# Kernel optimization log

Hardware: AMD Instinct MI355X
Metric: run time of the kernel (lower is better)

Reference implementation:

```python
import jax, jax.numpy as jnp
import numpy as np

SCALE = 100.0  # sharp-softmax temperature from the torch module

def _build_tables():
    # ByteToNibbleFFN: W1 is identity(256) so it is mathematically a no-op; keep W2.
    W2_b2n = np.zeros((256, 32), np.float32)
    bb = np.arange(256)
    W2_b2n[bb, bb >> 4] = 1.0
    W2_b2n[bb, 16 + (bb & 15)] = 1.0
    # NibbleAddWithCarryFFN tables
    W1_add = np.zeros((34, 512), np.float32)
    W2_sum = np.zeros((512, 16), np.float32)
    W2_cout = np.zeros((512, 2), np.float32)
    for a in range(16):
        for b in range(16):
            for c in range(2):
                idx = a * 32 + b * 2 + c
                W1_add[a, idx] = 1.0
                W1_add[16 + b, idx] = 1.0
                W1_add[32 + c, idx] = 1.0
                t = a + b + c
                W2_sum[idx, t & 15] = 1.0
                W2_cout[idx, 1 if t > 15 else 0] = 1.0
    # NibbleToByteFFN tables
    W1_n2b = np.zeros((32, 256), np.float32)
    W2_n2b = np.zeros((256, 256), np.float32)
    for h in range(16):
        for l in range(16):
            addr = h * 16 + l
            W1_n2b[h, addr] = 1.0
            W1_n2b[16 + l, addr] = 1.0
            W2_n2b[addr, (h << 4) | l] = 1.0
    return tuple(jnp.asarray(t) for t in (W2_b2n, W1_add, W2_sum, W2_cout, W1_n2b, W2_n2b))

W2_B2N, W1_ADD, W2_SUM, W2_COUT, W1_N2B, W2_N2B = _build_tables()

def _b2n(x):
    # byte [.,256] -> (high [.,16], low [.,16]); W1=eye(256) omitted (identity)
    out = x @ W2_B2N
    return out[..., :16], out[..., 16:]

def _nib_add(a, b, cin):
    combined = jnp.concatenate([a, b, cin], axis=-1)           # [.,34]
    address = jax.nn.softmax(combined @ W1_ADD * SCALE, axis=-1)  # [.,512]
    return address @ W2_SUM, address @ W2_COUT

def _n2b(high, low):
    combined = jnp.concatenate([high, low], axis=-1)           # [.,32]
    address = jax.nn.softmax(combined @ W1_N2B * SCALE, axis=-1)  # [.,256]
    return address @ W2_N2B

def setup_inputs() -> dict:
    key = jax.random.key(0)
    k1, k2 = jax.random.split(key)
    B = 32768
    a = jax.random.uniform(k1, (B, 4, 256), dtype=jnp.float32)
    b = jax.random.uniform(k2, (B, 4, 256), dtype=jnp.float32)
    return {"a": a, "b": b}

def reference(a, b):
    # NeuralALU.add: ripple-carry add over 4 bytes, 2 nibble adds per byte
    B = a.shape[0]
    carry = jnp.zeros((B, 2), a.dtype).at[:, 0].set(1.0)  # carry_zero one-hot
    out_bytes = []
    for i in range(4):  # fixed structural loop over bytes (carry dependence)
        ah, al = _b2n(a[:, i])
        bh, bl = _b2n(b[:, i])
        sl, carry = _nib_add(al, bl, carry)
        sh, carry = _nib_add(ah, bh, carry)
        out_bytes.append(_n2b(sh, sl))
    return jnp.stack(out_bytes, axis=1)  # [B,4,256]
```

## Files before the change

### kernel.cpp

```cpp
#include <hip/hip_runtime.h>

#define NIB_SCALE 100.0f

template<int CTRL>
__device__ __forceinline__ float fdpp(float x) {
    return __int_as_float(__builtin_amdgcn_update_dpp(
        0, __float_as_int(x), CTRL, 0xF, 0xF, true));
}

__device__ __forceinline__ float rsum16d(float v) {
    v += fdpp<0x121>(v); v += fdpp<0x122>(v); v += fdpp<0x124>(v); v += fdpp<0x128>(v);
    return v;
}
__device__ __forceinline__ float rmax16d(float v) {
    v = fmaxf(v, fdpp<0x121>(v)); v = fmaxf(v, fdpp<0x122>(v));
    v = fmaxf(v, fdpp<0x124>(v)); v = fmaxf(v, fdpp<0x128>(v));
    return v;
}
__device__ __forceinline__ float scan16d(float v) {
    v += fdpp<0x111>(v); v += fdpp<0x112>(v); v += fdpp<0x114>(v); v += fdpp<0x118>(v);
    return v;
}
__device__ __forceinline__ float softmax16d(float v) {
    float m = rmax16d(v);
    float e = __expf(NIB_SCALE * (v - m));
    float s = rsum16d(e);
    return e / s;
}
__device__ __forceinline__ float sharp_sigmoid(float c) {
    return 1.0f / (1.0f + __expf(NIB_SCALE * (1.0f - 2.0f * c)));
}

__device__ __forceinline__ float conv_quad(float g0, float g1, float g2, float g3,
                                           const float4 q) {
    return fmaf(g0, q.x, fmaf(g1, q.y, fmaf(g2, q.z, g3 * q.w)));
}

#define COLSUM_CHUNK(dst, r4, c)                                  \
    {                                                             \
        float s0 = rsum16d(r4.x), s1 = rsum16d(r4.y);             \
        float s2 = rsum16d(r4.z), s3 = rsum16d(r4.w);             \
        float t0 = (k & 1) ? s1 : s0;                             \
        float t1 = (k & 1) ? s3 : s2;                             \
        float tc = (k & 2) ? t1 : t0;                             \
        dst = ((k >> 2) == (c)) ? tc : dst;                       \
    }

__device__ __forceinline__ void carry_chain(const float4 O16L, const float4 O15L,
                                            const float4 O16H, const float4 O15H, int b,
                                            float& pc0, float& pc1, float& qc0, float& qc1) {
    float qc1_0 = sharp_sigmoid(O16L.x);
    float qc0_0 = 1.f - qc1_0;
    float pc1_1 = sharp_sigmoid(qc0_0 * O16H.x + qc1_0 * O15H.x);
    float pc0_1 = 1.f - pc1_1;
    float qc1_1 = sharp_sigmoid(pc0_1 * O16L.y + pc1_1 * O15L.y);
    float qc0_1 = 1.f - qc1_1;
    float pc1_2 = sharp_sigmoid(qc0_1 * O16H.y + qc1_1 * O15H.y);
    float pc0_2 = 1.f - pc1_2;
    float qc1_2 = sharp_sigmoid(pc0_2 * O16L.z + pc1_2 * O15L.z);
    float qc0_2 = 1.f - qc1_2;
    float pc1_3 = sharp_sigmoid(qc0_2 * O16H.z + qc1_2 * O15H.z);
    float pc0_3 = 1.f - pc1_3;
    float qc1_3 = sharp_sigmoid(pc0_3 * O16L.w + pc1_3 * O15L.w);
    float qc0_3 = 1.f - qc1_3;
    pc0 = b == 0 ? 1.f   : b == 1 ? pc0_1 : b == 2 ? pc0_2 : pc0_3;
    pc1 = b == 0 ? 0.f   : b == 1 ? pc1_1 : b == 2 ? pc1_2 : pc1_3;
    qc0 = b == 0 ? qc0_0 : b == 1 ? qc0_1 : b == 2 ? qc0_2 : qc0_3;
    qc1 = b == 0 ? qc1_0 : b == 1 ? qc1_1 : b == 2 ? qc1_2 : qc1_3;
}

__global__ void nalu_kernel(const float* __restrict__ A,
                            const float* __restrict__ B,
                            float* __restrict__ O,
                            int nrows) {
    __shared__ __align__(16) float sQL[16][16];
    __shared__ __align__(16) float sQH[16][16];
    __shared__ __align__(16) float sPSL[16][16];
    __shared__ __align__(16) float sPSH[16][16];
    __shared__ __align__(16) float sOV[4][4][4];

    const int tid = threadIdx.x;
    const int k = tid & 15;
    const int g = tid >> 4;
    const int b = g & 3;
    const int w = tid >> 6;
    constexpr int ROWS = 4;
    const int row0 = blockIdx.x * (4 * ROWS) + w * ROWS;
    if (row0 >= nrows) return;
    long base = (long)row0 * 1024 + b * 256;

    const float4* pa4 = (const float4*)(A + base + 16 * k);
    const float4* pb4 = (const float4*)(B + base + 16 * k);
    float4 ra0 = pa4[0], ra1 = pa4[1], ra2 = pa4[2], ra3 = pa4[3];
    float4 rb0 = pb4[0], rb1 = pb4[1], rb2 = pb4[2], rb3 = pb4[3];

    #pragma unroll
    for (int i = 0; i < ROWS; ++i) {
        if (row0 + i >= nrows) break;
        const bool more = (i + 1 < ROWS) && (row0 + i + 1 < nrows);
        const long nbase = more ? base + 1024 : base;

        const float4* na4 = (const float4*)(A + nbase + 16 * k);
        const float4* nb4 = (const float4*)(B + nbase + 16 * k);
        float4 xa0 = na4[0], xa1 = na4[1], xa2 = na4[2], xa3 = na4[3];
        float4 xb0 = nb4[0], xb1 = nb4[1], xb2 = nb4[2], xb3 = nb4[3];

        float ah = ((ra0.x + ra0.y) + (ra0.z + ra0.w)) + ((ra1.x + ra1.y) + (ra1.z + ra1.w))
                 + ((ra2.x + ra2.y) + (ra2.z + ra2.w)) + ((ra3.x + ra3.y) + (ra3.z + ra3.w));
        float bh = ((rb0.x + rb0.y) + (rb0.z + rb0.w)) + ((rb1.x + rb1.y) + (rb1.z + rb1.w))
                 + ((rb2.x + rb2.y) + (rb2.z + rb2.w)) + ((rb3.x + rb3.y) + (rb3.z + rb3.w));
        float al = 0.f, bl = 0.f;
        COLSUM_CHUNK(al, ra0, 0) COLSUM_CHUNK(al, ra1, 1)
        COLSUM_CHUNK(al, ra2, 2) COLSUM_CHUNK(al, ra3, 3)
        COLSUM_CHUNK(bl, rb0, 0) COLSUM_CHUNK(bl, rb1, 1)
        COLSUM_CHUNK(bl, rb2, 2) COLSUM_CHUNK(bl, rb3, 3)

        __builtin_amdgcn_sched_barrier(0);

        float pal = softmax16d(al);
        float pbl = softmax16d(bl);
        float pah = softmax16d(ah);
        float pbh = softmax16d(bh);

        sQL[g][k] = pbl;
        sQH[g][k] = pbh;

        float mirl = fdpp<0x140>(pbl);
        float mirh = fdpp<0x140>(pbh);
        float T15l = scan16d(mirl);
        float T15h = scan16d(mirh);
        float ov15l = rsum16d(pal * T15l);
        float c15l  = rsum16d(pal * mirl);
        float ov15h = rsum16d(pah * T15h);
        float c15h  = rsum16d(pah * mirh);

        sOV[w][0][b] = ov15l - c15l;
        sOV[w][1][b] = ov15l;
        sOV[w][2][b] = ov15h - c15h;
        sOV[w][3][b] = ov15h;

        const float4 La = *(const float4*)&sQL[g][0];
        const float4 Lb = *(const float4*)&sQL[g][4];
        const float4 Lc = *(const float4*)&sQL[g][8];
        const float4 Ld = *(const float4*)&sQL[g][12];
        float rl = (conv_quad(pal,              fdpp<0x121>(pal), fdpp<0x122>(pal), fdpp<0x123>(pal), La)
                  + conv_quad(fdpp<0x124>(pal), fdpp<0x125>(pal), fdpp<0x126>(pal), fdpp<0x127>(pal), Lb))
                 + (conv_quad(fdpp<0x128>(pal), fdpp<0x129>(pal), fdpp<0x12A>(pal), fdpp<0x12B>(pal), Lc)
                  + conv_quad(fdpp<0x12C>(pal), fdpp<0x12D>(pal), fdpp<0x12E>(pal), fdpp<0x12F>(pal), Ld));

        const float4 Ha = *(const float4*)&sQH[g][0];
        const float4 Hb = *(const float4*)&sQH[g][4];
        const float4 Hc = *(const float4*)&sQH[g][8];
        const float4 Hd = *(const float4*)&sQH[g][12];
        float rh = (conv_quad(pah,              fdpp<0x121>(pah), fdpp<0x122>(pah), fdpp<0x123>(pah), Ha)
                  + conv_quad(fdpp<0x124>(pah), fdpp<0x125>(pah), fdpp<0x126>(pah), fdpp<0x127>(pah), Hb))
                 + (conv_quad(fdpp<0x128>(pah), fdpp<0x129>(pah), fdpp<0x12A>(pah), fdpp<0x12B>(pah), Hc)
                  + conv_quad(fdpp<0x12C>(pah), fdpp<0x12D>(pah), fdpp<0x12E>(pah), fdpp<0x12F>(pah), Hd));

        float pc0, pc1, qc0, qc1;
        carry_chain(*(const float4*)&sOV[w][0][0], *(const float4*)&sOV[w][1][0],
                    *(const float4*)&sOV[w][2][0], *(const float4*)&sOV[w][3][0],
                    b, pc0, pc1, qc0, qc1);

        float slow  = pc0 * rl + pc1 * fdpp<0x121>(rl);
        float shigh = qc0 * rh + qc1 * fdpp<0x121>(rh);

        float psl = softmax16d(slow);
        float psh = softmax16d(shigh);
        sPSL[g][k] = psl;
        sPSH[g][k] = psh;

        const float4 pslq = *(const float4*)&sPSL[g][4 * (k & 3)];
        float* po = O + base;
        #pragma unroll
        for (int c = 0; c < 4; ++c) {
            float hs = sPSH[g][4 * c + (k >> 2)];
            *(float4*)(po + 64 * c + 4 * k) =
                make_float4(hs * pslq.x, hs * pslq.y, hs * pslq.z, hs * pslq.w);
        }

        ra0 = xa0; ra1 = xa1; ra2 = xa2; ra3 = xa3;
        rb0 = xb0; rb1 = xb1; rb2 = xb2; rb3 = xb3;
        base = nbase;
    }
}

extern "C" void kernel_launch(void* const* d_in, const int* in_sizes, int n_in,
                              void* d_out, int out_size, void* d_ws, size_t ws_size,
                              hipStream_t stream) {
    const float* A = (const float*)d_in[0];
    const float* B = (const float*)d_in[1];
    float* O = (float*)d_out;
    int nrows = in_sizes[0] / 1024;
    int grid = (nrows + 15) / 16;
    nalu_kernel<<<grid, 256, 0, stream>>>(A, B, O, nrows);
}
```

Baseline: 315.1 us.

## Process two rows per wave with upfront loads, readlane carry chain, direct low-nibble sums

Each wave now handles two rows, and all loads for both rows are issued before any compute, in place of a four-row software-pipelined loop. The low-nibble sums are read with strided scalar loads instead of DPP column reductions, and the carry-chain inputs are broadcast with readlane instead of a shared-memory round trip. The final softmax uses a fixed max of 0.5 rather than a computed max, and occupancy is pinned to four waves per EU. This trades extra global load instructions and a numerically riskier softmax for less cross-lane reduction and LDS traffic.

```diff
diff --git a/kernel.cpp b/kernel.cpp
--- a/kernel.cpp
+++ b/kernel.cpp
@@ -27,8 +27,16 @@
     float s = rsum16d(e);
     return e / s;
 }
+__device__ __forceinline__ float softmax16_fix(float v) {
+    float e = __expf(NIB_SCALE * (v - 0.5f));
+    float s = rsum16d(e);
+    return e / s;
+}
 __device__ __forceinline__ float sharp_sigmoid(float c) {
     return 1.0f / (1.0f + __expf(NIB_SCALE * (1.0f - 2.0f * c)));
+}
+__device__ __forceinline__ float rdlane(float x, int l) {
+    return __int_as_float(__builtin_amdgcn_readlane(__float_as_int(x), l));
 }
 
 __device__ __forceinline__ float conv_quad(float g0, float g1, float g2, float g3,
@@ -36,153 +44,160 @@
     return fmaf(g0, q.x, fmaf(g1, q.y, fmaf(g2, q.z, g3 * q.w)));
 }
 
-#define COLSUM_CHUNK(dst, r4, c)                                  \
-    {                                                             \
-        float s0 = rsum16d(r4.x), s1 = rsum16d(r4.y);             \
-        float s2 = rsum16d(r4.z), s3 = rsum16d(r4.w);             \
-        float t0 = (k & 1) ? s1 : s0;                             \
-        float t1 = (k & 1) ? s3 : s2;                             \
-        float tc = (k & 2) ? t1 : t0;                             \
-        dst = ((k >> 2) == (c)) ? tc : dst;                       \
+__device__ __forceinline__ void stream_tail(float al, float bl, float ah, float bh,
+                                            int k, int g, int b,
+                                            float (&QL)[16][16], float (&QH)[16][16],
+                                            float (&PSL)[16][16], float (&PSH)[16][16],
+                                            float* __restrict__ po) {
+    float pal = softmax16d(al);
+    float pbl = softmax16d(bl);
+    float pah = softmax16d(ah);
+    float pbh = softmax16d(bh);
+
+    QL[g][k] = pbl;
+    QH[g][k] = pbh;
+
+    float mirl = fdpp<0x140>(pbl);
+    float mirh = fdpp<0x140>(pbh);
+    float T15l = scan16d(mirl);
+    float T15h = scan16d(mirh);
+    float ov15l = rsum16d(pal * T15l);
+    float c15l  = rsum16d(pal * mirl);
+    float ov15h = rsum16d(pah * T15h);
+    float c15h  = rsum16d(pah * mirh);
+    float ov16l = ov15l - c15l;
+    float ov16h = ov15h - c15h;
+
+    float l16[4] = { rdlane(ov16l,0), rdlane(ov16l,16), rdlane(ov16l,32), rdlane(ov16l,48) };
+    float l15[4] = { rdlane(ov15l,0), rdlane(ov15l,16), rdlane(ov15l,32), rdlane(ov15l,48) };
+    float h16[4] = { rdlane(ov16h,0), rdlane(ov16h,16), rdlane(ov16h,32), rdlane(ov16h,48) };
+    float h15[4] = { rdlane(ov15h,0), rdlane(ov15h,16), rdlane(ov15h,32), rdlane(ov15h,48) };
+
+    const float4 La = *(const float4*)&QL[g][0];
+    const float4 Lb = *(const float4*)&QL[g][4];
+    const float4 Lc = *(const float4*)&QL[g][8];
+    const float4 Ld = *(const float4*)&QL[g][12];
+    float rl = (conv_quad(pal,              fdpp<0x121>(pal), fdpp<0x122>(pal), fdpp<0x123>(pal), La)
+              + conv_quad(fdpp<0x124>(pal), fdpp<0x125>(pal), fdpp<0x126>(pal), fdpp<0x127>(pal), Lb))
+             + (conv_quad(fdpp<0x128>(pal), fdpp<0x129>(pal), fdpp<0x12A>(pal), fdpp<0x12B>(pal), Lc)
+              + conv_quad(fdpp<0x12C>(pal), fdpp<0x12D>(pal), fdpp<0x12E>(pal), fdpp<0x12F>(pal), Ld));
+
+    const float4 Ha = *(const float4*)&QH[g][0];
+    const float4 Hb = *(const float4*)&QH[g][4];
+    const float4 Hc = *(const float4*)&QH[g][8];
+    const float4 Hd = *(const float4*)&QH[g][12];
+    float rh = (conv_quad(pah,              fdpp<0x121>(pah), fdpp<0x122>(pah), fdpp<0x123>(pah), Ha)
+              + conv_quad(fdpp<0x124>(pah), fdpp<0x125>(pah), fdpp<0x126>(pah), fdpp<0x127>(pah), Hb))
+             + (conv_quad(fdpp<0x128>(pah), fdpp<0x129>(pah), fdpp<0x12A>(pah), fdpp<0x12B>(pah), Hc)
+              + conv_quad(fdpp<0x12C>(pah), fdpp<0x12D>(pah), fdpp<0x12E>(pah), fdpp<0x12F>(pah), Hd));
+
+    float qc1_0 = sharp_sigmoid(l16[0]);
+    float qc0_0 = 1.f - qc1_0;
+    float pc1_1 = sharp_sigmoid(qc0_0 * h16[0] + qc1_0 * h15[0]);
+    float pc0_1 = 1.f - pc1_1;
+    float qc1_1 = sharp_sigmoid(pc0_1 * l16[1] + pc1_1 * l15[1]);
+    float qc0_1 = 1.f - qc1_1;
+    float pc1_2 = sharp_sigmoid(qc0_1 * h16[1] + qc1_1 * h15[1]);
+    float pc0_2 = 1.f - pc1_2;
+    float qc1_2 = sharp_sigmoid(pc0_2 * l16[2] + pc1_2 * l15[2]);
+    float qc0_2 = 1.f - qc1_2;
+    float pc1_3 = sharp_sigmoid(qc0_2 * h16[2] + qc1_2 * h15[2]);
+    float pc0_3 = 1.f - pc1_3;
+    float qc1_3 = sharp_sigmoid(pc0_3 * l16[3] + pc1_3 * l15[3]);
+    float qc0_3 = 1.f - qc1_3;
+
+    float pc0 = b == 0 ? 1.f   : b == 1 ? pc0_1 : b == 2 ? pc0_2 : pc0_3;
+    float pc1 = b == 0 ? 0.f   : b == 1 ? pc1_1 : b == 2 ? pc1_2 : pc1_3;
+    float qc0 = b == 0 ? qc0_0 : b == 1 ? qc0_1 : b == 2 ? qc0_2 : qc0_3;
+    float qc1 = b == 0 ? qc1_0 : b == 1 ? qc1_1 : b == 2 ? qc1_2 : qc1_3;
+
+    float slow  = pc0 * rl + pc1 * fdpp<0x121>(rl);
+    float shigh = qc0 * rh + qc1 * fdpp<0x121>(rh);
+
+    float psl = softmax16_fix(slow);
+    float psh = softmax16_fix(shigh);
+    PSL[g][k] = psl;
+    PSH[g][k] = psh;
+
+    const float4 pslq = *(const float4*)&PSL[g][4 * (k & 3)];
+    #pragma unroll
+    for (int c = 0; c < 4; ++c) {
+        float hs = PSH[g][4 * c + (k >> 2)];
+        *(float4*)(po + 64 * c + 4 * k) =
+            make_float4(hs * pslq.x, hs * pslq.y, hs * pslq.z, hs * pslq.w);
     }
-
-__device__ __forceinline__ void carry_chain(const float4 O16L, const float4 O15L,
-                                            const float4 O16H, const float4 O15H, int b,
-                                            float& pc0, float& pc1, float& qc0, float& qc1) {
-    float qc1_0 = sharp_sigmoid(O16L.x);
-    float qc0_0 = 1.f - qc1_0;
-    float pc1_1 = sharp_sigmoid(qc0_0 * O16H.x + qc1_0 * O15H.x);
-    float pc0_1 = 1.f - pc1_1;
-    float qc1_1 = sharp_sigmoid(pc0_1 * O16L.y + pc1_1 * O15L.y);
-    float qc0_1 = 1.f - qc1_1;
-    float pc1_2 = sharp_sigmoid(qc0_1 * O16H.y + qc1_1 * O15H.y);
-    float pc0_2 = 1.f - pc1_2;
-    float qc1_2 = sharp_sigmoid(pc0_2 * O16L.z + pc1_2 * O15L.z);
-    float qc0_2 = 1.f - qc1_2;
-    float pc1_3 = sharp_sigmoid(qc0_2 * O16H.z + qc1_2 * O15H.z);
-    float pc0_3 = 1.f - pc1_3;
-    float qc1_3 = sharp_sigmoid(pc0_3 * O16L.w + pc1_3 * O15L.w);
-    float qc0_3 = 1.f - qc1_3;
-    pc0 = b == 0 ? 1.f   : b == 1 ? pc0_1 : b == 2 ? pc0_2 : pc0_3;
-    pc1 = b == 0 ? 0.f   : b == 1 ? pc1_1 : b == 2 ? pc1_2 : pc1_3;
-    qc0 = b == 0 ? qc0_0 : b == 1 ? qc0_1 : b == 2 ? qc0_2 : qc0_3;
-    qc1 = b == 0 ? qc1_0 : b == 1 ? qc1_1 : b == 2 ? qc1_2 : qc1_3;
-}
-
-__global__ void nalu_kernel(const float* __restrict__ A,
-                            const float* __restrict__ B,
-                            float* __restrict__ O,
-                            int nrows) {
-    __shared__ __align__(16) float sQL[16][16];
-    __shared__ __align__(16) float sQH[16][16];
-    __shared__ __align__(16) float sPSL[16][16];
-    __shared__ __align__(16) float sPSH[16][16];
-    __shared__ __align__(16) float sOV[4][4][4];
+}
+
+__global__ __launch_bounds__(256)
+__attribute__((amdgpu_waves_per_eu(4, 4)))
+void nalu_kernel(const float* __restrict__ A,
+                 const float* __restrict__ B,
+                 float* __restrict__ O,
+                 int nrows) {
+    __shared__ __align__(16) float sQL[2][16][16];
+    __shared__ __align__(16) float sQH[2][16][16];
+    __shared__ __align__(16) float sPSL[2][16][16];
+    __shared__ __align__(16) float sPSH[2][16][16];
 
     const int tid = threadIdx.x;
     const int k = tid & 15;
     const int g = tid >> 4;
     const int b = g & 3;
     const int w = tid >> 6;
-    constexpr int ROWS = 4;
-    const int row0 = blockIdx.x * (4 * ROWS) + w * ROWS;
+    const int row0 = blockIdx.x * 8 + w * 2;
     if (row0 >= nrows) return;
-    long base = (long)row0 * 1024 + b * 256;
-
-    const float4* pa4 = (const float4*)(A + base + 16 * k);
-    const float4* pb4 = (const float4*)(B + base + 16 * k);
-    float4 ra0 = pa4[0], ra1 = pa4[1], ra2 = pa4[2], ra3 = pa4[3];
-    float4 rb0 = pb4[0], rb1 = pb4[1], rb2 = pb4[2], rb3 = pb4[3];
-
+    const long base0 = (long)row0 * 1024 + b * 256;
+    const long base1 = base0 + ((row0 + 1 < nrows) ? 1024 : 0);
+
+    const float* pa0 = A + base0;  const float* pb0 = B + base0;
+    const float* pa1 = A + base1;  const float* pb1 = B + base1;
+
+    const float4* qa0 = (const float4*)(pa0 + 16 * k);
+    const float4* qb0 = (const float4*)(pb0 + 16 * k);
+    const float4* qa1 = (const float4*)(pa1 + 16 * k);
+    const float4* qb1 = (const float4*)(pb1 + 16 * k);
+    float4 ra0 = qa0[0], ra1 = qa0[1], ra2 = qa0[2], ra3 = qa0[3];
+    float4 rb0 = qb0[0], rb1 = qb0[1], rb2 = qb0[2], rb3 = qb0[3];
+    float4 sa0 = qa1[0], sa1 = qa1[1], sa2 = qa1[2], sa3 = qa1[3];
+    float4 sb0 = qb1[0], sb1 = qb1[1], sb2 = qb1[2], sb3 = qb1[3];
+
+    float uA0 = 0, uA1 = 0, uA2 = 0, uA3 = 0, uB0 = 0, uB1 = 0, uB2 = 0, uB3 = 0;
     #pragma unroll
-    for (int i = 0; i < ROWS; ++i) {
-        if (row0 + i >= nrows) break;
-        const bool more = (i + 1 < ROWS) && (row0 + i + 1 < nrows);
-        const long nbase = more ? base + 1024 : base;
-
-        const float4* na4 = (const float4*)(A + nbase + 16 * k);
-        const float4* nb4 = (const float4*)(B + nbase + 16 * k);
-        float4 xa0 = na4[0], xa1 = na4[1], xa2 = na4[2], xa3 = na4[3];
-        float4 xb0 = nb4[0], xb1 = nb4[1], xb2 = nb4[2], xb3 = nb4[3];
-
-        float ah = ((ra0.x + ra0.y) + (ra0.z + ra0.w)) + ((ra1.x + ra1.y) + (ra1.z + ra1.w))
-                 + ((ra2.x + ra2.y) + (ra2.z + ra2.w)) + ((ra3.x + ra3.y) + (ra3.z + ra3.w));
-        float bh = ((rb0.x + rb0.y) + (rb0.z + rb0.w)) + ((rb1.x + rb1.y) + (rb1.z + rb1.w))
-                 + ((rb2.x + rb2.y) + (rb2.z + rb2.w)) + ((rb3.x + rb3.y) + (rb3.z + rb3.w));
-        float al = 0.f, bl = 0.f;
-        COLSUM_CHUNK(al, ra0, 0) COLSUM_CHUNK(al, ra1, 1)
-        COLSUM_CHUNK(al, ra2, 2) COLSUM_CHUNK(al, ra3, 3)
-        COLSUM_CHUNK(bl, rb0, 0) COLSUM_CHUNK(bl, rb1, 1)
-        COLSUM_CHUNK(bl, rb2, 2) COLSUM_CHUNK(bl, rb3, 3)
-
-        __builtin_amdgcn_sched_barrier(0);
-
-        float pal = softmax16d(al);
-        float pbl = softmax16d(bl);
-        float pah = softmax16d(ah);
-        float pbh = softmax16d(bh);
-
-        sQL[g][k] = pbl;
-        sQH[g][k] = pbh;
-
-        float mirl = fdpp<0x140>(pbl);
-        float mirh = fdpp<0x140>(pbh);
-        float T15l = scan16d(mirl);
-        float T15h = scan16d(mirh);
-        float ov15l = rsum16d(pal * T15l);
-        float c15l  = rsum16d(pal * mirl);
-        float ov15h = rsum16d(pah * T15h);
-        float c15h  = rsum16d(pah * mirh);
-
-        sOV[w][0][b] = ov15l - c15l;
-        sOV[w][1][b] = ov15l;
-        sOV[w][2][b] = ov15h - c15h;
-        sOV[w][3][b] = ov15h;
-
-        const float4 La = *(const float4*)&sQL[g][0];
-        const float4 Lb = *(const float4*)&sQL[g][4];
-        const float4 Lc = *(const float4*)&sQL[g][8];
-        const float4 Ld = *(const float4*)&sQL[g][12];
-        float rl = (conv_quad(pal,              fdpp<0x121>(pal), fdpp<0x122>(pal), fdpp<0x123>(pal), La)
-                  + conv_quad(fdpp<0x124>(pal), fdpp<0x125>(pal), fdpp<0x126>(pal), fdpp<0x127>(pal), Lb))
-                 + (conv_quad(fdpp<0x128>(pal), fdpp<0x129>(pal), fdpp<0x12A>(pal), fdpp<0x12B>(pal), Lc)
-                  + conv_quad(fdpp<0x12C>(pal), fdpp<0x12D>(pal), fdpp<0x12E>(pal), fdpp<0x12F>(pal), Ld));
-
-        const float4 Ha = *(const float4*)&sQH[g][0];
-        const float4 Hb = *(const float4*)&sQH[g][4];
-        const float4 Hc = *(const float4*)&sQH[g][8];
-        const float4 Hd = *(const float4*)&sQH[g][12];
-        float rh = (conv_quad(pah,              fdpp<0x121>(pah), fdpp<0x122>(pah), fdpp<0x123>(pah), Ha)
-                  + conv_quad(fdpp<0x124>(pah), fdpp<0x125>(pah), fdpp<0x126>(pah), fdpp<0x127>(pah), Hb))
-                 + (conv_quad(fdpp<0x128>(pah), fdpp<0x129>(pah), fdpp<0x12A>(pah), fdpp<0x12B>(pah), Hc)
-                  + conv_quad(fdpp<0x12C>(pah), fdpp<0x12D>(pah), fdpp<0x12E>(pah), fdpp<0x12F>(pah), Hd));
-
-        float pc0, pc1, qc0, qc1;
-        carry_chain(*(const float4*)&sOV[w][0][0], *(const float4*)&sOV[w][1][0],
-                    *(const float4*)&sOV[w][2][0], *(const float4*)&sOV[w][3][0],
-                    b, pc0, pc1, qc0, qc1);
-
-        float slow  = pc0 * rl + pc1 * fdpp<0x121>(rl);
-        float shigh = qc0 * rh + qc1 * fdpp<0x121>(rh);
-
-        float psl = softmax16d(slow);
-        float psh = softmax16d(shigh);
-        sPSL[g][k] = psl;
-        sPSH[g][k] = psh;
-
-        const float4 pslq = *(const float4*)&sPSL[g][4 * (k & 3)];
-        float* po = O + base;
-        #pragma unroll
-        for (int c = 0; c < 4; ++c) {
-            float hs = sPSH[g][4 * c + (k >> 2)];
-            *(float4*)(po + 64 * c + 4 * k) =
-                make_float4(hs * pslq.x, hs * pslq.y, hs * pslq.z, hs * pslq.w);
-        }
-
-        ra0 = xa0; ra1 = xa1; ra2 = xa2; ra3 = xa3;
-        rb0 = xb0; rb1 = xb1; rb2 = xb2; rb3 = xb3;
-        base = nbase;
+    for (int e = 0; e < 4; ++e) {
+        uA0 += pa0[16 * e + k];        uB0 += pb0[16 * e + k];
+        uA1 += pa0[16 * (e + 4) + k];  uB1 += pb0[16 * (e + 4) + k];
+        uA2 += pa0[16 * (e + 8) + k];  uB2 += pb0[16 * (e + 8) + k];
+        uA3 += pa0[16 * (e + 12) + k]; uB3 += pb0[16 * (e + 12) + k];
     }
+
+    float al0 = (uA0 + uA1) + (uA2 + uA3);
+    float bl0 = (uB0 + uB1) + (uB2 + uB3);
+    float ah0 = ((ra0.x + ra0.y) + (ra0.z + ra0.w)) + ((ra1.x + ra1.y) + (ra1.z + ra1.w))
+              + ((ra2.x + ra2.y) + (ra2.z + ra2.w)) + ((ra3.x + ra3.y) + (ra3.z + ra3.w));
+    float bh0 = ((rb0.x + rb0.y) + (rb0.z + rb0.w)) + ((rb1.x + rb1.y) + (rb1.z + rb1.w))
+              + ((rb2.x + rb2.y) + (rb2.z + rb2.w)) + ((rb3.x + rb3.y) + (rb3.z + rb3.w));
+
+    float vA0 = 0, vA1 = 0, vA2 = 0, vA3 = 0, vB0 = 0, vB1 = 0, vB2 = 0, vB3 = 0;
+    #pragma unroll
+    for (int e = 0; e < 4; ++e) {
+        vA0 += pa1[16 * e + k];        vB0 += pb1[16 * e + k];
+        vA1 += pa1[16 * (e + 4) + k];  vB1 += pb1[16 * (e + 4) + k];
+        vA2 += pa1[16 * (e + 8) + k];  vB2 += pb1[16 * (e + 8) + k];
+        vA3 += pa1[16 * (e + 12) + k]; vB3 += pb1[16 * (e + 12) + k];
+    }
+
+    __builtin_amdgcn_sched_barrier(0);
+
+    stream_tail(al0, bl0, ah0, bh0, k, g, b, sQL[0], sQH[0], sPSL[0], sPSH[0], O + base0);
+
+    float al1 = (vA0 + vA1) + (vA2 + vA3);
+    float bl1 = (vB0 + vB1) + (vB2 + vB3);
+    float ah1 = ((sa0.x + sa0.y) + (sa0.z + sa0.w)) + ((sa1.x + sa1.y) + (sa1.z + sa1.w))
+              + ((sa2.x + sa2.y) + (sa2.z + sa2.w)) + ((sa3.x + sa3.y) + (sa3.z + sa3.w));
+    float bh1 = ((sb0.x + sb0.y) + (sb0.z + sb0.w)) + ((sb1.x + sb1.y) + (sb1.z + sb1.w))
+              + ((sb2.x + sb2.y) + (sb2.z + sb2.w)) + ((sb3.x + sb3.y) + (sb3.z + sb3.w));
+
+    stream_tail(al1, bl1, ah1, bh1, k, g, b, sQL[1], sQH[1], sPSL[1], sPSH[1], O + base1);
 }
 
 extern "C" void kernel_launch(void* const* d_in, const int* in_sizes, int n_in,
@@ -192,6 +207,6 @@
     const float* B = (const float*)d_in[1];
     float* O = (float*)d_out;
     int nrows = in_sizes[0] / 1024;
-    int grid = (nrows + 15) / 16;
+    int grid = (nrows + 7) / 8;
     nalu_kernel<<<grid, 256, 0, stream>>>(A, B, O, nrows);
 }
```

New measurement: 312.6 us. No clear change (-0.8%).
